# Optimization experiments

Measured on AMD Instinct MI355X. Metric: run time of the kernel, lower is better.

## Reference

```python
import jax, jax.numpy as jnp
import numpy as np

INTERVENTION_STRENGTH = 1.0


def setup_inputs() -> dict:
    key = jax.random.key(0)
    k1, k2, k3 = jax.random.split(key, 3)
    B, n_regimes, d = 256, 16, 512
    A_per_env = jax.random.normal(k1, (B, d, d), dtype=jnp.float32)
    intervention_mask = (jax.random.uniform(k2, (n_regimes, d)) < 0.1).astype(jnp.float32)
    regimes = jax.random.randint(k3, (B,), 0, n_regimes, dtype=jnp.int64)
    return {"A_per_env": A_per_env, "intervention_mask": intervention_mask, "regimes": regimes}


def reference(A_per_env, intervention_mask, regimes):
    # A_per_env: [B, d, d], intervention_mask: [n_regimes, d], regimes: [B] int
    n_regimes = intervention_mask.shape[0]
    valid = (regimes < n_regimes)                                   # [B] skip out-of-range regimes
    e = jnp.clip(regimes, 0, n_regimes - 1)
    masks = intervention_mask[e] * valid[:, None].astype(intervention_mask.dtype)  # [B, d] gather
    incoming = A_per_env.sum(axis=1)                                # [B, d] sum over source nodes
    loss = jnp.sum(incoming * masks)
    count = jnp.sum(masks)                                          # total intervened-node count
    loss = jnp.where(count > 0, loss / count, loss)
    # original returns exactly 0.0 when the mask is globally empty (holds here since masks==0)
    return INTERVENTION_STRENGTH * loss
```

## Files before the change

### kernel.cpp

```cpp
#include <hip/hip_runtime.h>

constexpr int D      = 512;
constexpr int D4     = D / 4;
constexpr int CHUNKS = 8;
constexpr int BLOCK  = 256;
constexpr int F4_PER_CHUNK = (D * D / 4) / CHUNKS;
constexpr int ITERS  = F4_PER_CHUNK / BLOCK;

__global__ __launch_bounds__(BLOCK) void iw_loss_kernel(
    const float* __restrict__ A,
    const float* __restrict__ mask,
    const int*  __restrict__ regimes,
    int n_regimes,
    double* __restrict__ ws)
{
    const int b     = blockIdx.x / CHUNKS;
    const int chunk = blockIdx.x % CHUNKS;
    const int tid   = threadIdx.x;

    __shared__ float4 smask[D4];
    const int r = regimes[b];
    const int e = r < 0 ? 0 : (r >= n_regimes ? n_regimes - 1 : r);
    const float v = (r < n_regimes) ? 1.0f : 0.0f;
    if (tid < D4) {
        float4 m = reinterpret_cast<const float4*>(mask + (size_t)e * D)[tid];
        m.x *= v; m.y *= v; m.z *= v; m.w *= v;
        smask[tid] = m;
    }
    __syncthreads();

    const float4* A4 = reinterpret_cast<const float4*>(A) + (size_t)b * (D * D / 4);
    const float4 m = smask[tid & (D4 - 1)];

    float acc = 0.0f;
    const int f0 = chunk * F4_PER_CHUNK + tid;
    #pragma unroll
    for (int it = 0; it < ITERS; ++it) {
        const float4 a = A4[f0 + it * BLOCK];
        acc = fmaf(a.x, m.x, acc);
        acc = fmaf(a.y, m.y, acc);
        acc = fmaf(a.z, m.z, acc);
        acc = fmaf(a.w, m.w, acc);
    }

    #pragma unroll
    for (int off = 32; off > 0; off >>= 1)
        acc += __shfl_down(acc, off, 64);

    __shared__ double wsum[BLOCK / 64];
    if ((tid & 63) == 0) wsum[tid >> 6] = (double)acc;
    __syncthreads();
    if (tid == 0) {
        double s = 0.0;
        #pragma unroll
        for (int w = 0; w < BLOCK / 64; ++w) s += wsum[w];
        atomicAdd(ws, s);
    }
}

__global__ __launch_bounds__(256) void iw_finalize_kernel(
    const float* __restrict__ mask,
    const int*  __restrict__ regimes,
    int n_regimes, int B,
    const double* __restrict__ ws,
    float* __restrict__ out)
{
    __shared__ float rowsum[64];
    const int tid = threadIdx.x;

    const int row = tid >> 4;
    const int seg = tid & 15;
    float s = 0.0f;
    if (row < n_regimes) {
        const float4* m4 = reinterpret_cast<const float4*>(mask + (size_t)row * D);
        #pragma unroll
        for (int k = 0; k < D4 / 16; ++k) {
            const float4 m = m4[seg + k * 16];
            s += m.x + m.y + m.z + m.w;
        }
    }
    #pragma unroll
    for (int off = 8; off > 0; off >>= 1) s += __shfl_down(s, off, 16);
    if (seg == 0 && row < n_regimes) rowsum[row] = s;
    __syncthreads();

    float cf = 0.0f;
    for (int b = tid; b < B; b += 256) {
        const int r = regimes[b];
        if (r < n_regimes) cf += rowsum[r < 0 ? 0 : r];
    }
    #pragma unroll
    for (int off = 32; off > 0; off >>= 1) cf += __shfl_down(cf, off, 64);

    __shared__ double csum[4];
    if ((tid & 63) == 0) csum[tid >> 6] = (double)cf;
    __syncthreads();
    if (tid == 0) {
        const double count = csum[0] + csum[1] + csum[2] + csum[3];
        const double loss  = ws[0];
        out[0] = (float)(count > 0.0 ? loss / count : loss);
    }
}

extern "C" void kernel_launch(void* const* d_in, const int* in_sizes, int n_in,
                              void* d_out, int out_size, void* d_ws, size_t ws_size,
                              hipStream_t stream) {
    const float* A       = (const float*)d_in[0];
    const float* mask    = (const float*)d_in[1];
    const int*   regimes = (const int*)d_in[2];
    const int B          = in_sizes[2];
    const int n_regimes  = in_sizes[1] / D;
    double* ws = (double*)d_ws;

    hipMemsetAsync(d_ws, 0, sizeof(double), stream);
    iw_loss_kernel<<<B * CHUNKS, BLOCK, 0, stream>>>(A, mask, regimes, n_regimes, ws);
    iw_finalize_kernel<<<1, 256, 0, stream>>>(mask, regimes, n_regimes, B, ws,
                                              (float*)d_out);
}
```

Baseline: 363.5 us.

## Replace atomic accumulation with per-block partials and use nontemporal loads

Each block now writes its partial sum to its own workspace slot, and the finalize kernel reduces those slots. This removes the global double atomic and the memset launch. The mask is read straight from global memory instead of being staged in shared memory, which drops one barrier. The A stream uses nontemporal loads batched four at a time to raise memory-level parallelism. The trade-off is extra workspace traffic and a serial partial reduction in the single-block finalize kernel.

```diff
diff --git a/kernel.cpp b/kernel.cpp
--- a/kernel.cpp
+++ b/kernel.cpp
@@ -7,75 +7,82 @@
 constexpr int F4_PER_CHUNK = (D * D / 4) / CHUNKS;
 constexpr int ITERS  = F4_PER_CHUNK / BLOCK;
 
+typedef float f32x4 __attribute__((ext_vector_type(4)));
+
 __global__ __launch_bounds__(BLOCK) void iw_loss_kernel(
     const float* __restrict__ A,
     const float* __restrict__ mask,
     const int*  __restrict__ regimes,
     int n_regimes,
-    double* __restrict__ ws)
+    double* __restrict__ partial)
 {
     const int b     = blockIdx.x / CHUNKS;
     const int chunk = blockIdx.x % CHUNKS;
     const int tid   = threadIdx.x;
 
-    __shared__ float4 smask[D4];
     const int r = regimes[b];
     const int e = r < 0 ? 0 : (r >= n_regimes ? n_regimes - 1 : r);
     const float v = (r < n_regimes) ? 1.0f : 0.0f;
-    if (tid < D4) {
-        float4 m = reinterpret_cast<const float4*>(mask + (size_t)e * D)[tid];
-        m.x *= v; m.y *= v; m.z *= v; m.w *= v;
-        smask[tid] = m;
-    }
-    __syncthreads();
 
-    const float4* A4 = reinterpret_cast<const float4*>(A) + (size_t)b * (D * D / 4);
-    const float4 m = smask[tid & (D4 - 1)];
+    f32x4 m = reinterpret_cast<const f32x4*>(mask + (size_t)e * D)[tid & (D4 - 1)];
+    m *= v;
+
+    const f32x4* A4 = reinterpret_cast<const f32x4*>(A)
+                    + (size_t)b * (D * D / 4) + chunk * F4_PER_CHUNK + tid;
 
     float acc = 0.0f;
-    const int f0 = chunk * F4_PER_CHUNK + tid;
     #pragma unroll
-    for (int it = 0; it < ITERS; ++it) {
-        const float4 a = A4[f0 + it * BLOCK];
-        acc = fmaf(a.x, m.x, acc);
-        acc = fmaf(a.y, m.y, acc);
-        acc = fmaf(a.z, m.z, acc);
-        acc = fmaf(a.w, m.w, acc);
+    for (int it = 0; it < ITERS; it += 4) {
+        const f32x4 a0 = __builtin_nontemporal_load(A4 + (it + 0) * BLOCK);
+        const f32x4 a1 = __builtin_nontemporal_load(A4 + (it + 1) * BLOCK);
+        const f32x4 a2 = __builtin_nontemporal_load(A4 + (it + 2) * BLOCK);
+        const f32x4 a3 = __builtin_nontemporal_load(A4 + (it + 3) * BLOCK);
+        acc = fmaf(a0.x, m.x, acc); acc = fmaf(a0.y, m.y, acc);
+        acc = fmaf(a0.z, m.z, acc); acc = fmaf(a0.w, m.w, acc);
+        acc = fmaf(a1.x, m.x, acc); acc = fmaf(a1.y, m.y, acc);
+        acc = fmaf(a1.z, m.z, acc); acc = fmaf(a1.w, m.w, acc);
+        acc = fmaf(a2.x, m.x, acc); acc = fmaf(a2.y, m.y, acc);
+        acc = fmaf(a2.z, m.z, acc); acc = fmaf(a2.w, m.w, acc);
+        acc = fmaf(a3.x, m.x, acc); acc = fmaf(a3.y, m.y, acc);
+        acc = fmaf(a3.z, m.z, acc); acc = fmaf(a3.w, m.w, acc);
     }
 
     #pragma unroll
     for (int off = 32; off > 0; off >>= 1)
         acc += __shfl_down(acc, off, 64);
 
-    __shared__ double wsum[BLOCK / 64];
-    if ((tid & 63) == 0) wsum[tid >> 6] = (double)acc;
+    __shared__ float wsum[BLOCK / 64];
+    if ((tid & 63) == 0) wsum[tid >> 6] = acc;
     __syncthreads();
     if (tid == 0) {
         double s = 0.0;
         #pragma unroll
-        for (int w = 0; w < BLOCK / 64; ++w) s += wsum[w];
-        atomicAdd(ws, s);
+        for (int w = 0; w < BLOCK / 64; ++w) s += (double)wsum[w];
+        partial[blockIdx.x] = s;
     }
 }
 
 __global__ __launch_bounds__(256) void iw_finalize_kernel(
     const float* __restrict__ mask,
     const int*  __restrict__ regimes,
-    int n_regimes, int B,
-    const double* __restrict__ ws,
+    int n_regimes, int B, int n_partial,
+    const double* __restrict__ partial,
     float* __restrict__ out)
 {
-    __shared__ float rowsum[64];
     const int tid = threadIdx.x;
 
+    double ls = 0.0;
+    for (int k = tid; k < n_partial; k += 256) ls += partial[k];
+
+    __shared__ float rowsum[64];
     const int row = tid >> 4;
     const int seg = tid & 15;
     float s = 0.0f;
     if (row < n_regimes) {
-        const float4* m4 = reinterpret_cast<const float4*>(mask + (size_t)row * D);
+        const f32x4* m4 = reinterpret_cast<const f32x4*>(mask + (size_t)row * D);
         #pragma unroll
         for (int k = 0; k < D4 / 16; ++k) {
-            const float4 m = m4[seg + k * 16];
+            const f32x4 m = m4[seg + k * 16];
             s += m.x + m.y + m.z + m.w;
         }
     }
@@ -89,15 +96,19 @@
         const int r = regimes[b];
         if (r < n_regimes) cf += rowsum[r < 0 ? 0 : r];
     }
+
     #pragma unroll
-    for (int off = 32; off > 0; off >>= 1) cf += __shfl_down(cf, off, 64);
-
-    __shared__ double csum[4];
-    if ((tid & 63) == 0) csum[tid >> 6] = (double)cf;
+    for (int off = 32; off > 0; off >>= 1) {
+        ls += __shfl_down(ls, off, 64);
+        cf += __shfl_down(cf, off, 64);
+    }
+    __shared__ double lsum[4];
+    __shared__ float  csum[4];
+    if ((tid & 63) == 0) { lsum[tid >> 6] = ls; csum[tid >> 6] = cf; }
     __syncthreads();
     if (tid == 0) {
-        const double count = csum[0] + csum[1] + csum[2] + csum[3];
-        const double loss  = ws[0];
+        const double loss  = lsum[0] + lsum[1] + lsum[2] + lsum[3];
+        const double count = (double)csum[0] + csum[1] + csum[2] + csum[3];
         out[0] = (float)(count > 0.0 ? loss / count : loss);
     }
 }
@@ -110,10 +121,10 @@
     const int*   regimes = (const int*)d_in[2];
     const int B          = in_sizes[2];
     const int n_regimes  = in_sizes[1] / D;
-    double* ws = (double*)d_ws;
+    double* partial = (double*)d_ws;
 
-    hipMemsetAsync(d_ws, 0, sizeof(double), stream);
-    iw_loss_kernel<<<B * CHUNKS, BLOCK, 0, stream>>>(A, mask, regimes, n_regimes, ws);
-    iw_finalize_kernel<<<1, 256, 0, stream>>>(mask, regimes, n_regimes, B, ws,
-                                              (float*)d_out);
+    const int nblocks = B * CHUNKS;
+    iw_loss_kernel<<<nblocks, BLOCK, 0, stream>>>(A, mask, regimes, n_regimes, partial);
+    iw_finalize_kernel<<<1, 256, 0, stream>>>(mask, regimes, n_regimes, B, nblocks,
+                                              partial, (float*)d_out);
 }
```

New measurement: 334.7 us. -7.9%, faster.
